# Kernel optimization log

Hardware: AMD Instinct MI355X
Metric: run time of the kernel (lower is better)

## Reference

```python
import jax, jax.numpy as jnp
import numpy as np

B, S, T = 64, 1024, 64
H, A, DA, DT, P, NT = 1024, 1024, 512, 256, 256, 32
DIN = DA + A + DT  # LSTMCell input: [a_tm1_embed, att_tm1, pre_type]


def setup_inputs() -> dict:
    key = jax.random.key(0)
    ks = jax.random.split(key, 16)
    nrm = lambda k, shape, s=0.02: jax.random.normal(k, shape, jnp.float32) * s
    return {
        'src_encodings': jax.random.normal(ks[0], (B, S, H), jnp.float32),
        'W_ih': nrm(ks[1], (4 * H, DIN)), 'b_ih': jnp.zeros((4 * H,), jnp.float32),
        'W_hh': nrm(ks[2], (4 * H, H)), 'b_hh': jnp.zeros((4 * H,), jnp.float32),
        'W_att': nrm(ks[3], (H, H)),            # att_sketch_linear (no bias)
        'W_attvec': nrm(ks[4], (A, 2 * H)),     # sketch_att_vec_linear (no bias)
        'W_init': nrm(ks[5], (H, H)), 'b_init': jnp.zeros((H,), jnp.float32),  # decoder_cell_init
        'W_q2a': nrm(ks[6], (DA, A)), 'b_q2a': jnp.zeros((DA,), jnp.float32),  # query_vec_to_action_embed
        'prod_embed': nrm(ks[7], (P, DA), 0.05), 'prod_bias': jnp.zeros((P,), jnp.float32),
        'type_embed': nrm(ks[8], (NT, DT), 0.05),
        'prev_prod_ids': jax.random.randint(ks[9], (B, T), 0, P),
        'prev_type_ids': jax.random.randint(ks[10], (B, T), 0, NT),
        'target_prod_ids': jax.random.randint(ks[11], (B, T), 0, P),
        'sketch_lens': jax.random.randint(ks[12], (B,), T // 2, T + 1),
        'src_lens': jax.random.randint(ks[13], (B,), S // 2, S + 1),
    }


def _lstm_cell(x, h, c, W_ih, b_ih, W_hh, b_hh):
    gates = x @ W_ih.T + b_ih + h @ W_hh.T + b_hh
    i, f, g, o = jnp.split(gates, 4, axis=-1)
    c_new = jax.nn.sigmoid(f) * c + jax.nn.sigmoid(i) * jnp.tanh(g)
    h_new = jax.nn.sigmoid(o) * jnp.tanh(c_new)
    return h_new, c_new


def reference(src_encodings, W_ih, b_ih, W_hh, b_hh, W_att, W_attvec, W_init, b_init,
              W_q2a, b_q2a, prod_embed, prod_bias, type_embed,
              prev_prod_ids, prev_type_ids, target_prod_ids, sketch_lens, src_lens):
    Bq, Sq, Hq = src_encodings.shape
    Tq = prev_prod_ids.shape[1]
    src_valid = jnp.arange(Sq)[None, :] < src_lens[:, None]            # [B,S] True = real token
    step_valid = jnp.arange(Tq)[None, :] < sketch_lens[:, None]        # [B,T]
    prev_valid = step_valid & (jnp.arange(Tq)[None, :] > 0)            # prev action exists

    src_att = jnp.einsum('bsh,kh->bsk', src_encodings, W_att)          # att_sketch_linear
    # init_decoder_state(adaptive_avg_pool1d(enc,1))
    init_cell = src_encodings.mean(axis=1)
    h0 = jnp.tanh(init_cell @ W_init.T + b_init)
    c0 = jnp.zeros_like(h0)
    att0 = jnp.zeros((Bq, A), src_encodings.dtype)

    # precomputed grammar lookups (production / type embeddings of a_{t-1})
    a_embeds = jnp.where(prev_valid[..., None], prod_embed[prev_prod_ids], 0.0)   # [B,T,DA]
    t_embeds = jnp.where(prev_valid[..., None], type_embed[prev_type_ids], 0.0)   # [B,T,DT]
    is_first = jnp.arange(Tq) == 0                                                # [T]

    def step(carry, inp):
        h, c, att_tm1 = carry
        a_e, t_e, first = inp
        x = jnp.concatenate([a_e, att_tm1, t_e], axis=-1)
        x = jnp.where(first, 0.0, x)                                   # t==0 -> zero input
        h, c = _lstm_cell(x, h, c, W_ih, b_ih, W_hh, b_hh)
        scores = jnp.einsum('bh,bsh->bs', h, src_att)
        scores = jnp.where(src_valid, scores, -1e9)
        alpha = jax.nn.softmax(scores, axis=-1)
        ctx = jnp.einsum('bs,bsh->bh', alpha, src_encodings)
        att_t = jnp.tanh(jnp.concatenate([h, ctx], axis=-1) @ W_attvec.T)
        q = jnp.tanh(att_t @ W_q2a.T + b_q2a)                          # non_linear readout
        probs = jax.nn.softmax(q @ prod_embed.T + prod_bias, axis=-1)  # [B,P]
        return (h, c, att_t), probs

    xs = (jnp.swapaxes(a_embeds, 0, 1), jnp.swapaxes(t_embeds, 0, 1), is_first)
    _, probs = jax.lax.scan(step, (h0, c0, att0), xs)                  # [T,B,P]

    tgt = jnp.swapaxes(target_prod_ids, 0, 1)[..., None]               # [T,B,1]
    p_t = jnp.take_along_axis(probs, tgt, axis=-1)[..., 0]             # [T,B]
    logp = jnp.log(p_t + 1e-8)
    sketch_prob = jnp.sum(jnp.where(step_valid.T, logp, 0.0), axis=0)  # [B]
    return sketch_prob
```

## Files before the change

### kernel.cpp

```cpp
#include <hip/hip_runtime.h>
#include <hip/hip_bf16.h>

typedef unsigned short u16;
typedef unsigned char u8;
typedef unsigned int u32;
typedef unsigned long long u64;
typedef __attribute__((ext_vector_type(8))) short short8;
typedef __attribute__((ext_vector_type(8))) u16 ushort8;
typedef __attribute__((ext_vector_type(4))) float f32x4;
typedef __attribute__((ext_vector_type(2))) float f32x2;

__device__ __forceinline__ float bf2f(u16 x){ u32 u=((u32)x)<<16; return __builtin_bit_cast(float,u); }
__device__ __forceinline__ u16 f2bf(float f){ u32 u=__builtin_bit_cast(u32,f); u32 r=(u+0x7fffu+((u>>16)&1u))>>16; return (u16)r; }
__device__ __forceinline__ float sigf(float x){ return 1.f/(1.f+__expf(-x)); }

__device__ __forceinline__ void scf(float* p, float v){
  __hip_atomic_store(p, v, __ATOMIC_RELAXED, __HIP_MEMORY_SCOPE_AGENT);
}
__device__ __forceinline__ void scu16(u16* p, u16 v){
  __hip_atomic_store(p, v, __ATOMIC_RELAXED, __HIP_MEMORY_SCOPE_AGENT);
}
__device__ __forceinline__ int ald(const int* p){
  return __hip_atomic_load(p, __ATOMIC_RELAXED, __HIP_MEMORY_SCOPE_AGENT);
}


__global__ __launch_bounds__(256) void k_cast(const float* __restrict__ s, u16* __restrict__ d, long n){
  long i = ((long)blockIdx.x*256 + threadIdx.x)*8;
  if (i >= n) return;
  float4 a = *(const float4*)(s+i);
  float4 b = *(const float4*)(s+i+4);
  ushort8 o;
  o[0]=f2bf(a.x); o[1]=f2bf(a.y); o[2]=f2bf(a.z); o[3]=f2bf(a.w);
  o[4]=f2bf(b.x); o[5]=f2bf(b.y); o[6]=f2bf(b.z); o[7]=f2bf(b.w);
  *(ushort8*)(d+i) = o;
}

__global__ __launch_bounds__(256) void k_cast8(const float* __restrict__ s, u8* __restrict__ d, long n){
  long i = ((long)blockIdx.x*256 + threadIdx.x)*8;
  if (i >= n) return;
  float4 a = *(const float4*)(s+i);
  float4 b = *(const float4*)(s+i+4);
  u32 w0 = 0, w1 = 0;
  w0 = __builtin_amdgcn_cvt_pk_fp8_f32(a.x, a.y, w0, false);
  w0 = __builtin_amdgcn_cvt_pk_fp8_f32(a.z, a.w, w0, true);
  w1 = __builtin_amdgcn_cvt_pk_fp8_f32(b.x, b.y, w1, false);
  w1 = __builtin_amdgcn_cvt_pk_fp8_f32(b.z, b.w, w1, true);
  uint2 o; o.x = w0; o.y = w1;
  *(uint2*)(d+i) = o;
}

__global__ __launch_bounds__(256) void k_build_wc(const float* __restrict__ Wih, const float* __restrict__ Whh,
                                                  u16* __restrict__ WC){
  long i8 = (long)blockIdx.x*256 + threadIdx.x;
  if (i8 >= (long)4096*352) return;
  int j = (int)(i8/352); int kk = (int)(i8%352)*8;
  const float* src;
  if (kk < 512)        src = Wih + (long)j*1792 + kk;
  else if (kk < 768)   src = Wih + (long)j*1792 + (kk+1024);
  else if (kk < 1792)  src = Wih + (long)j*1792 + (kk-256);
  else                 src = Whh + (long)j*1024 + (kk-1792);
  u16* dst = WC + (long)j*2816 + kk;
  ushort8 o;
  #pragma unroll
  for (int q=0;q<8;++q) o[q] = f2bf(src[q]);
  *(ushort8*)dst = o;
}

__global__ __launch_bounds__(256) void k_wattT(const float* __restrict__ Wa, u16* __restrict__ WT){
  int id = blockIdx.x*256 + threadIdx.x;
  int m = id >> 10, k = id & 1023;
  WT[(long)m*1024 + k] = f2bf(Wa[(long)k*1024 + m]);
}

__global__ __launch_bounds__(256) void k_meanf(const float* __restrict__ enc, u16* __restrict__ MEANB){
  int b = blockIdx.x, h = blockIdx.y*256 + threadIdx.x;
  const float* p = enc + ((long)b<<20) + h;
  float s = 0.f;
  for (int ss=0; ss<1024; ++ss) s += p[(long)ss<<10];
  MEANB[b*1024 + h] = f2bf(s * (1.f/1024.f));
}

__global__ __launch_bounds__(256) void k_embed(const float* __restrict__ pemb, const float* __restrict__ temb,
      const int* __restrict__ pid, const int* __restrict__ tid_, const int* __restrict__ slen,
      u16* __restrict__ XC){
  int t = blockIdx.x >> 6, b = blockIdx.x & 63;
  bool valid = (t>0) && (t < slen[b]);
  int pi = pid[b*64 + t], ti = tid_[b*64 + t];
  u16* dst = XC + (long)blockIdx.x*2816;
  for (int kk = threadIdx.x; kk < 768; kk += 256){
    float v = 0.f;
    if (valid) v = (kk<512) ? pemb[(long)pi*512 + kk] : temb[(long)ti*256 + (kk-512)];
    dst[kk] = f2bf(v);
  }
}

template<int MODE>
__global__ __launch_bounds__(256) void k_gemm(const u16* __restrict__ A, long lda,
      const u16* __restrict__ W, int K, const float* __restrict__ bias,
      float* __restrict__ OF, long ldo, u16* __restrict__ OB1, long ldb1){
  int l = threadIdx.x & 63, w = threadIdx.x >> 6;
  int c = l & 15, g = l >> 4;
  int n0 = blockIdx.x*16, m0 = blockIdx.y*64;
  const u16* ap = A + (long)(m0 + w*16 + c)*lda + g*8;
  const u16* bp = W + (long)(n0 + c)*K + g*8;
  f32x4 acc = {0.f,0.f,0.f,0.f};
  int kit = K >> 5;
  #pragma unroll 4
  for (int kb=0; kb<kit; ++kb){
    short8 av = *(const short8*)(ap + kb*32);
    short8 bv = *(const short8*)(bp + kb*32);
    acc = __builtin_amdgcn_mfma_f32_16x16x32_bf16(av, bv, acc, 0, 0, 0);
  }
  #pragma unroll
  for (int r=0;r<4;++r){
    int row = m0 + w*16 + g*4 + r;
    int col = n0 + c;
    float v = acc[r];
    if (MODE==2){ OB1[(long)row*ldb1 + col] = f2bf(tanhf(v + bias[col])); }
    if (MODE==3){ OF[(long)row*ldo + col] = v + bias[col]; }
  }
}

__global__ __launch_bounds__(256) void k_loss(const float* __restrict__ LG, const int* __restrict__ tgt,
      const int* __restrict__ slen, float* __restrict__ out){
  int b = blockIdx.x;
  int w = threadIdx.x >> 6, l = threadIdx.x & 63;
  int len = slen[b];
  float accum = 0.f;
  for (int t = w; t < 64; t += 4){
    if (t >= len) continue;
    const float* lp = LG + ((long)(t*64 + b))*256;
    float v0=lp[l], v1=lp[l+64], v2=lp[l+128], v3=lp[l+192];
    float mx = fmaxf(fmaxf(v0,v1), fmaxf(v2,v3));
    #pragma unroll
    for (int off=32; off; off>>=1) mx = fmaxf(mx, __shfl_xor(mx, off));
    float s = __expf(v0-mx)+__expf(v1-mx)+__expf(v2-mx)+__expf(v3-mx);
    #pragma unroll
    for (int off=32; off; off>>=1) s += __shfl_xor(s, off);
    float ltg = lp[tgt[b*64 + t]];
    float p = __expf(ltg - mx)/s;
    accum += logf(p + 1e-8f);
  }
  __shared__ float sm[4];
  if (l == 0) sm[w] = accum;
  __syncthreads();
  if (threadIdx.x == 0) out[b] = sm[0]+sm[1]+sm[2]+sm[3];
}

__device__ __forceinline__ void gbar(int* __restrict__ BAR, int gen){
  int grp = blockIdx.x & 15;
  int prev = __hip_atomic_fetch_add(BAR + grp*16, 1, __ATOMIC_RELAXED, __HIP_MEMORY_SCOPE_AGENT);
  if (prev == gen*16 - 1){
    int p2 = __hip_atomic_fetch_add(BAR + 256, 1, __ATOMIC_RELAXED, __HIP_MEMORY_SCOPE_AGENT);
    if (p2 == gen*16 - 1){
      #pragma unroll
      for (int i=0;i<16;++i)
        __hip_atomic_store(BAR + 320 + i*16, gen, __ATOMIC_RELAXED, __HIP_MEMORY_SCOPE_AGENT);
    }
  }
  while (ald(BAR + 320 + grp*16) < gen)
    __builtin_amdgcn_s_sleep(2);
}

__global__ __launch_bounds__(1024,1) void k_decoder(
      const u8* __restrict__ ENC8, const u16* __restrict__ WC,
      const u16* __restrict__ WAVT, const u16* __restrict__ WAVEC,
      const float* __restrict__ bih, const float* __restrict__ bhh,
      u16* __restrict__ XC, u16* __restrict__ ATT,
      float* __restrict__ HWT, float* __restrict__ PLT,
      u16* __restrict__ CTXBT, const int* __restrict__ src_lens,
      int* __restrict__ BAR){
  const int tid = threadIdx.x;
  const int w = tid >> 6, l = tid & 63, c = l & 15, g = l >> 4;
  const int bx = blockIdx.x;
  int genb = 0;

  __shared__ float smem[12320];
  f32x4* lacc  = (f32x4*)smem;
  float* s_ctx = smem;
  float* s_ls  = smem + 12288;
  u16*   ldsc  = (u16*)smem;
  f32x4* lacc4 = (f32x4*)(smem + 8192);

  const int n0 = bx << 2;
  const int jrow = n0 + (c & 3) + ((c >> 2) << 10);
  const float biasj = bih[jrow] + bhh[jrow];
  const int kh = w >> 2, mt = w & 3;
  const int lbase = l & 0x33;
  float creg[4] = {0.f,0.f,0.f,0.f};
  const int mt2 = bx & 3, nt2 = bx >> 2;
  const int b3 = bx >> 2, ci3 = bx & 3;
  int len3 = src_lens[b3]; if (len3 < 1) len3 = 1; if (len3 > 1024) len3 = 1024;
  const int chunk3 = (len3 + 3) >> 2;
  int s0 = ci3*chunk3;
  int s1 = s0 + chunk3; if (s1 > len3) s1 = len3;
  const u8* encb = ENC8 + (((long)b3)<<20);
  int lim = s1 - s0 - w;
  int nqv = (lim <= 0) ? 0 : ((lim + 15) >> 4);
  if (nqv > 16) nqv = 16;
  const int mt4 = bx & 3, nt4 = bx >> 2;
  const int b16 = tid >> 6, lane64 = tid & 63;

  uint4 er[12];
  #pragma unroll
  for (int q=0;q<12;++q){
    int r = s0 + q*16 + w;
    if (r >= s1) r = s0;
    er[q] = *(const uint4*)(encb + ((long)r<<10) + l*16);
  }

  for (int t = 0; t < 64; ++t){
    const u16* XCt = XC + (size_t)t*64*2816;
    u16* XCn = XC + (size_t)(t+1)*64*2816;
    const u16* Hcur = XCn + 1792;
    float* HW   = HWT  + ((size_t)t<<16);
    float* PL   = PLT  + ((size_t)t<<8);
    u16*  CTXB  = CTXBT + ((size_t)t<<18);

    {
      const u16* ap = XCt + (long)(mt*16 + c)*2816 + kh*704 + g*8;
      const u16* bp = WC  + (long)jrow*2816 + kh*704 + g*8;
      f32x4 acc = {0.f,0.f,0.f,0.f};
      #pragma unroll 11
      for (int kb=0; kb<22; ++kb){
        short8 av = *(const short8*)(ap + kb*32);
        short8 bv = *(const short8*)(bp + kb*32);
        acc = __builtin_amdgcn_mfma_f32_16x16x32_bf16(av, bv, acc, 0, 0, 0);
      }
      lacc[w*64 + l] = acc;
      __syncthreads();
      if (w < 4){
        f32x4 a0 = lacc[w*64 + l];
        f32x4 a1 = lacc[(w+4)*64 + l];
        f32x4 a2 = lacc[(w+8)*64 + l];
        f32x4 a3 = lacc[(w+12)*64 + l];
        #pragma unroll
        for (int r=0;r<4;++r){
          float val = a0[r] + a1[r] + a2[r] + a3[r] + biasj;
          float iv = __shfl(val, lbase);
          float fv = __shfl(val, lbase+4);
          float gv = __shfl(val, lbase+8);
          float ov = __shfl(val, lbase+12);
          if ((l & 12) == 0){
            float cn = sigf(fv)*creg[r] + sigf(iv)*tanhf(gv);
            float hn = sigf(ov)*tanhf(cn);
            creg[r] = cn;
            int b = w*16 + g*4 + r;
            int n = n0 + (l & 3);
            scu16(XCn + (long)b*2816 + 1792 + n, f2bf(hn));
          }
        }
      }
    }
    ++genb;
    __syncthreads();
    if (tid == 0) gbar(BAR, genb);
    __syncthreads();

    {
      const u16* ap = Hcur + (long)(mt2*16 + c)*2816 + w*64 + g*8;
      const u16* bp = WAVT + (long)(nt2*16 + c)*1024 + w*64 + g*8;
      f32x4 acc = {0.f,0.f,0.f,0.f};
      #pragma unroll
      for (int kb=0; kb<2; ++kb){
        short8 av = *(const short8*)(ap + kb*32);
        short8 bv = *(const short8*)(bp + kb*32);
        acc = __builtin_amdgcn_mfma_f32_16x16x32_bf16(av, bv, acc, 0, 0, 0);
      }
      lacc[w*64 + l] = acc;
      __syncthreads();
      if (w == 0){
        f32x4 rd = lacc[l];
        #pragma unroll
        for (int w2=1; w2<16; ++w2) rd += lacc[w2*64 + l];
        #pragma unroll
        for (int r=0;r<4;++r)
          scf(HW + (long)(mt2*16 + g*4 + r)*1024 + nt2*16 + c, rd[r]);
      }
    }
    ++genb;
    __syncthreads();
    if (tid == 0) gbar(BAR, genb);
    __syncthreads();

    {
      float hw[16], ctx[16];
      const float* hwp = HW + b3*1024 + l*16;
      #pragma unroll
      for (int jj=0;jj<4;++jj){
        float4 v = *(const float4*)(hwp + jj*4);
        hw[4*jj]=v.x; hw[4*jj+1]=v.y; hw[4*jj+2]=v.z; hw[4*jj+3]=v.w;
      }
      #pragma unroll
      for (int jj=0;jj<16;++jj) ctx[jj]=0.f;
      float lsum = 0.f;
      auto proc = [&](uint4 ev){
        float e[16];
        #pragma unroll
        for (int jj=0;jj<4;++jj){
          u32 x = ((const u32*)&ev)[jj];
          f32x2 lo = __builtin_amdgcn_cvt_pk_f32_fp8(x, false);
          f32x2 hi = __builtin_amdgcn_cvt_pk_f32_fp8(x, true);
          e[4*jj]=lo[0]; e[4*jj+1]=lo[1]; e[4*jj+2]=hi[0]; e[4*jj+3]=hi[1];
        }
        float sc = 0.f;
        #pragma unroll
        for (int jj=0;jj<16;++jj) sc += e[jj]*hw[jj];
        #pragma unroll
        for (int off=32; off; off>>=1) sc += __shfl_xor(sc, off);
        float pe = __expf(sc);
        lsum += pe;
        #pragma unroll
        for (int jj=0;jj<16;++jj) ctx[jj] += pe*e[jj];
      };
      #pragma unroll
      for (int q=0;q<12;++q) if (q < nqv) proc(er[q]);
      for (int q=12; q<nqv; ++q){
        uint4 ev = *(const uint4*)(encb + ((long)(s0 + q*16 + w)<<10) + l*16);
        proc(ev);
      }
      if (l == 0) s_ls[w] = lsum;
      if (w < 8){
        #pragma unroll
        for (int jj=0;jj<16;++jj) s_ctx[w*1024 + l*16 + jj] = ctx[jj];
      }
      __syncthreads();
      if (w >= 8){
        #pragma unroll
        for (int jj=0;jj<16;++jj) s_ctx[(w-8)*1024 + l*16 + jj] += ctx[jj];
      }
      __syncthreads();
      {
        float v = 0.f;
        #pragma unroll
        for (int p=0;p<8;++p) v += s_ctx[p*1024 + tid];
        scu16(CTXB + (((long)bx)<<10) + tid, f2bf(v));
      }
      if (tid == 0){
        float L = 0.f;
        #pragma unroll
        for (int q=0;q<16;++q) L += s_ls[q];
        scf(PL + bx, L);
      }
    }
    ++genb;
    __syncthreads();
    if (tid == 0) gbar(BAR, genb);
    __syncthreads();

    {
      int b = mt4*16 + b16;
      float L = PL[b*4] + PL[b*4+1] + PL[b*4+2] + PL[b*4+3];
      float inv = (L > 0.f) ? 1.f/L : 0.f;
      const u16* r0 = CTXB + (long)(b*4+0)*1024;
      const u16* r1 = CTXB + (long)(b*4+1)*1024;
      const u16* r2 = CTXB + (long)(b*4+2)*1024;
      const u16* r3 = CTXB + (long)(b*4+3)*1024;
      const int swz = (b16 & 7) << 3;
      #pragma unroll
      for (int q=0;q<2;++q){
        int mcol8 = (lane64 + q*64)*8;
        ushort8 v0 = *(const ushort8*)(r0 + mcol8);
        ushort8 v1 = *(const ushort8*)(r1 + mcol8);
        ushort8 v2 = *(const ushort8*)(r2 + mcol8);
        ushort8 v3 = *(const ushort8*)(r3 + mcol8);
        ushort8 o;
        #pragma unroll
        for (int j=0;j<8;++j)
          o[j] = f2bf((bf2f(v0[j]) + bf2f(v1[j]) + bf2f(v2[j]) + bf2f(v3[j])) * inv);
        *(ushort8*)(ldsc + ((b16*1024 + mcol8) ^ swz)) = o;
      }
      __syncthreads();
      f32x4 acc = {0.f,0.f,0.f,0.f};
      const int koff = (w < 8) ? w*128 : 1024 + (w-8)*128;
      const u16* bp = WAVEC + (long)(nt4*16 + c)*2048 + koff + g*8;
      if (w < 8){
        const u16* ap = Hcur + (long)(mt4*16 + c)*2816 + w*128 + g*8;
        #pragma unroll
        for (int kb=0; kb<4; ++kb){
          short8 av = *(const short8*)(ap + kb*32);
          short8 bv = *(const short8*)(bp + kb*32);
          acc = __builtin_amdgcn_mfma_f32_16x16x32_bf16(av, bv, acc, 0, 0, 0);
        }
      } else {
        const int cswz = (c & 7) << 3;
        const int kbase = c*1024 + (w-8)*128 + g*8;
        #pragma unroll
        for (int kb=0; kb<4; ++kb){
          short8 av = *(const short8*)(ldsc + ((kbase + kb*32) ^ cswz));
          short8 bv = *(const short8*)(bp + kb*32);
          acc = __builtin_amdgcn_mfma_f32_16x16x32_bf16(av, bv, acc, 0, 0, 0);
        }
      }
      lacc4[w*64 + l] = acc;
      __syncthreads();
      if (w == 0){
        f32x4 rd = lacc4[l];
        #pragma unroll
        for (int w2=1; w2<16; ++w2) rd += lacc4[w2*64 + l];
        #pragma unroll
        for (int r=0;r<4;++r){
          int b_ = mt4*16 + g*4 + r;
          int col = nt4*16 + c;
          u16 x = f2bf(tanhf(rd[r]));
          scu16(XCn + (long)b_*2816 + 768 + col, x);
          ATT[((long)t*64 + b_)*1024 + col] = x;
        }
      }
    }
    ++genb;
    __syncthreads();
    if (tid == 0) gbar(BAR, genb);
    __syncthreads();
  }
}

extern "C" void kernel_launch(void* const* d_in, const int* in_sizes, int n_in,
                              void* d_out, int out_size, void* d_ws, size_t ws_size,
                              hipStream_t stream){
  const float* enc      = (const float*)d_in[0];
  const float* W_ih     = (const float*)d_in[1];
  const float* b_ih     = (const float*)d_in[2];
  const float* W_hh     = (const float*)d_in[3];
  const float* b_hh     = (const float*)d_in[4];
  const float* W_att    = (const float*)d_in[5];
  const float* W_attvec = (const float*)d_in[6];
  const float* W_init   = (const float*)d_in[7];
  const float* b_init   = (const float*)d_in[8];
  const float* W_q2a    = (const float*)d_in[9];
  const float* b_q2a    = (const float*)d_in[10];
  const float* prod_emb = (const float*)d_in[11];
  const float* prod_bias= (const float*)d_in[12];
  const float* type_emb = (const float*)d_in[13];
  const int* prev_pid   = (const int*)d_in[14];
  const int* prev_tid   = (const int*)d_in[15];
  const int* target     = (const int*)d_in[16];
  const int* sk_lens    = (const int*)d_in[17];
  const int* src_lens   = (const int*)d_in[18];
  float* out = (float*)d_out;

  char* ws = (char*)d_ws;
  size_t o = 0;
  auto alloc = [&](size_t bytes)->char*{ char* p = ws + o; o += (bytes + 255) & ~(size_t)255; return p; };
  u8*   ENC8 = (u8*)alloc((size_t)64*1024*1024);
  u16*  WC   = (u16*)alloc((size_t)4096*2816*2);
  u16*  WAVT = (u16*)alloc((size_t)1024*1024*2);
  u16*  WAVEC= (u16*)alloc((size_t)1024*2048*2);
  u16*  WQ   = (u16*)alloc((size_t)512*1024*2);
  u16*  PE   = (u16*)alloc((size_t)256*512*2);
  u16*  WINIT= (u16*)alloc((size_t)1024*1024*2);
  u16*  MEANB= (u16*)alloc((size_t)64*1024*2);
  u16*  XC   = (u16*)alloc((size_t)65*64*2816*2);
  u16*  ATT  = (u16*)alloc((size_t)64*64*1024*2);
  float* HWT = (float*)alloc((size_t)64*64*1024*4);
  float* PLT = (float*)alloc((size_t)64*256*4);
  u16*  CTXBT=(u16*)alloc((size_t)64*256*1024*2);
  u16*  Q    = (u16*)alloc((size_t)4096*512*2);
  float* LG  = (float*)alloc((size_t)4096*256*4);
  int*  BAR  = (int*)alloc(4096);
  (void)ws_size; (void)in_sizes; (void)n_in; (void)out_size;

  hipMemsetAsync(XC, 0, (size_t)64*2816*2, stream);
  hipMemsetAsync(BAR, 0, 4096, stream);

  k_cast8<<<32768,256,0,stream>>>(enc, ENC8, (long)64*1024*1024);
  k_cast<<<1024,256,0,stream>>>(W_attvec, WAVEC, (long)1024*2048);
  k_cast<<<256,256,0,stream>>>(W_q2a, WQ, (long)512*1024);
  k_cast<<<64,256,0,stream>>>(prod_emb, PE, (long)256*512);
  k_cast<<<512,256,0,stream>>>(W_init, WINIT, (long)1024*1024);
  k_build_wc<<<5632,256,0,stream>>>(W_ih, W_hh, WC);
  k_wattT<<<4096,256,0,stream>>>(W_att, WAVT);
  k_meanf<<<dim3(64,4),256,0,stream>>>(enc, MEANB);
  k_gemm<2><<<dim3(64,1),256,0,stream>>>(MEANB, 1024L, WINIT, 1024, b_init,
                                         nullptr, 0L, XC + 1792, 2816L);
  k_embed<<<4096,256,0,stream>>>(prod_emb, type_emb, prev_pid, prev_tid, sk_lens, XC);

  k_decoder<<<256,1024,0,stream>>>(ENC8, WC, WAVT, WAVEC, b_ih, b_hh,
                                   XC, ATT, HWT, PLT, CTXBT, src_lens, BAR);

  k_gemm<2><<<dim3(32,64),256,0,stream>>>(ATT, 1024L, WQ, 1024, b_q2a,
                                          nullptr, 0L, Q, 512L);
  k_gemm<3><<<dim3(16,64),256,0,stream>>>(Q, 512L, PE, 512, prod_bias,
                                          LG, 256L, nullptr, 0L);
  k_loss<<<64,256,0,stream>>>(LG, target, sk_lens, out);
}
```

Baseline: 3.868 ms.

## Partition decoder blocks into four batch groups with independent 64-block barriers

Reassigns work so each group of 64 blocks owns 16 batch rows end to end (LSTM gates, attention projection, context, attention vector), which lets the grid barrier be replaced by four independent 64-block barriers instead of one 256-block barrier. The aim is to cut barrier latency and contention per step. In exchange, each block now reads the full weight rows for its slice while handling fewer batch rows, so the weights are read four times as often. The attention output store also becomes an atomic relaxed store.

```diff
diff --git a/kernel.cpp b/kernel.cpp
--- a/kernel.cpp
+++ b/kernel.cpp
@@ -148,18 +148,18 @@
   if (threadIdx.x == 0) out[b] = sm[0]+sm[1]+sm[2]+sm[3];
 }
 
-__device__ __forceinline__ void gbar(int* __restrict__ BAR, int gen){
-  int grp = blockIdx.x & 15;
-  int prev = __hip_atomic_fetch_add(BAR + grp*16, 1, __ATOMIC_RELAXED, __HIP_MEMORY_SCOPE_AGENT);
-  if (prev == gen*16 - 1){
-    int p2 = __hip_atomic_fetch_add(BAR + 256, 1, __ATOMIC_RELAXED, __HIP_MEMORY_SCOPE_AGENT);
-    if (p2 == gen*16 - 1){
-      #pragma unroll
-      for (int i=0;i<16;++i)
-        __hip_atomic_store(BAR + 320 + i*16, gen, __ATOMIC_RELAXED, __HIP_MEMORY_SCOPE_AGENT);
+__device__ __forceinline__ void gbar64(int* __restrict__ B, int gen, int sub){
+  int g8 = sub & 7;
+  int prev = __hip_atomic_fetch_add(B + g8*16, 1, __ATOMIC_RELAXED, __HIP_MEMORY_SCOPE_AGENT);
+  if (prev == gen*8 - 1){
+    int p2 = __hip_atomic_fetch_add(B + 128, 1, __ATOMIC_RELAXED, __HIP_MEMORY_SCOPE_AGENT);
+    if (p2 == gen*8 - 1){
+      #pragma unroll
+      for (int i=0;i<8;++i)
+        __hip_atomic_store(B + 160 + i*16, gen, __ATOMIC_RELAXED, __HIP_MEMORY_SCOPE_AGENT);
     }
   }
-  while (ald(BAR + 320 + grp*16) < gen)
+  while (ald(B + 160 + g8*16) < gen)
     __builtin_amdgcn_s_sleep(2);
 }
 
@@ -174,6 +174,8 @@
   const int tid = threadIdx.x;
   const int w = tid >> 6, l = tid & 63, c = l & 15, g = l >> 4;
   const int bx = blockIdx.x;
+  const int grpid = bx >> 6, sub = bx & 63, bg0 = grpid << 4;
+  int* BARg = BAR + grpid*1024;
   int genb = 0;
 
   __shared__ float smem[12320];
@@ -183,14 +185,12 @@
   u16*   ldsc  = (u16*)smem;
   f32x4* lacc4 = (f32x4*)(smem + 8192);
 
-  const int n0 = bx << 2;
-  const int jrow = n0 + (c & 3) + ((c >> 2) << 10);
+  const int ns = w & 3, kh = w >> 2;
+  const int jrow = sub*16 + ns*4 + (c & 3) + ((c >> 2) << 10);
   const float biasj = bih[jrow] + bhh[jrow];
-  const int kh = w >> 2, mt = w & 3;
   const int lbase = l & 0x33;
   float creg[4] = {0.f,0.f,0.f,0.f};
-  const int mt2 = bx & 3, nt2 = bx >> 2;
-  const int b3 = bx >> 2, ci3 = bx & 3;
+  const int b3 = bg0 + (sub >> 2), ci3 = sub & 3;
   int len3 = src_lens[b3]; if (len3 < 1) len3 = 1; if (len3 > 1024) len3 = 1024;
   const int chunk3 = (len3 + 3) >> 2;
   int s0 = ci3*chunk3;
@@ -199,7 +199,6 @@
   int lim = s1 - s0 - w;
   int nqv = (lim <= 0) ? 0 : ((lim + 15) >> 4);
   if (nqv > 16) nqv = 16;
-  const int mt4 = bx & 3, nt4 = bx >> 2;
   const int b16 = tid >> 6, lane64 = tid & 63;
 
   uint4 er[12];
@@ -219,7 +218,7 @@
     u16*  CTXB  = CTXBT + ((size_t)t<<18);
 
     {
-      const u16* ap = XCt + (long)(mt*16 + c)*2816 + kh*704 + g*8;
+      const u16* ap = XCt + (long)(bg0 + c)*2816 + kh*704 + g*8;
       const u16* bp = WC  + (long)jrow*2816 + kh*704 + g*8;
       f32x4 acc = {0.f,0.f,0.f,0.f};
       #pragma unroll 11
@@ -246,8 +245,8 @@
             float cn = sigf(fv)*creg[r] + sigf(iv)*tanhf(gv);
             float hn = sigf(ov)*tanhf(cn);
             creg[r] = cn;
-            int b = w*16 + g*4 + r;
-            int n = n0 + (l & 3);
+            int b = bg0 + g*4 + r;
+            int n = sub*16 + w*4 + (l & 3);
             scu16(XCn + (long)b*2816 + 1792 + n, f2bf(hn));
           }
         }
@@ -255,12 +254,12 @@
     }
     ++genb;
     __syncthreads();
-    if (tid == 0) gbar(BAR, genb);
+    if (tid == 0) gbar64(BARg, genb, sub);
     __syncthreads();
 
     {
-      const u16* ap = Hcur + (long)(mt2*16 + c)*2816 + w*64 + g*8;
-      const u16* bp = WAVT + (long)(nt2*16 + c)*1024 + w*64 + g*8;
+      const u16* ap = Hcur + (long)(bg0 + c)*2816 + w*64 + g*8;
+      const u16* bp = WAVT + (long)(sub*16 + c)*1024 + w*64 + g*8;
       f32x4 acc = {0.f,0.f,0.f,0.f};
       #pragma unroll
       for (int kb=0; kb<2; ++kb){
@@ -276,17 +275,17 @@
         for (int w2=1; w2<16; ++w2) rd += lacc[w2*64 + l];
         #pragma unroll
         for (int r=0;r<4;++r)
-          scf(HW + (long)(mt2*16 + g*4 + r)*1024 + nt2*16 + c, rd[r]);
+          scf(HW + (long)(bg0 + g*4 + r)*1024 + sub*16 + c, rd[r]);
       }
     }
     ++genb;
     __syncthreads();
-    if (tid == 0) gbar(BAR, genb);
+    if (tid == 0) gbar64(BARg, genb, sub);
     __syncthreads();
 
     {
       float hw[16], ctx[16];
-      const float* hwp = HW + b3*1024 + l*16;
+      const float* hwp = HW + (long)b3*1024 + l*16;
       #pragma unroll
       for (int jj=0;jj<4;++jj){
         float4 v = *(const float4*)(hwp + jj*4);
@@ -346,17 +345,18 @@
     }
     ++genb;
     __syncthreads();
-    if (tid == 0) gbar(BAR, genb);
+    if (tid == 0) gbar64(BARg, genb, sub);
     __syncthreads();
 
     {
-      int b = mt4*16 + b16;
-      float L = PL[b*4] + PL[b*4+1] + PL[b*4+2] + PL[b*4+3];
+      int pb = grpid*64 + b16*4;
+      float4 plv = *(const float4*)(PL + pb);
+      float L = plv.x + plv.y + plv.z + plv.w;
       float inv = (L > 0.f) ? 1.f/L : 0.f;
-      const u16* r0 = CTXB + (long)(b*4+0)*1024;
-      const u16* r1 = CTXB + (long)(b*4+1)*1024;
-      const u16* r2 = CTXB + (long)(b*4+2)*1024;
-      const u16* r3 = CTXB + (long)(b*4+3)*1024;
+      const u16* r0 = CTXB + ((long)(pb+0)<<10);
+      const u16* r1 = CTXB + ((long)(pb+1)<<10);
+      const u16* r2 = CTXB + ((long)(pb+2)<<10);
+      const u16* r3 = CTXB + ((long)(pb+3)<<10);
       const int swz = (b16 & 7) << 3;
       #pragma unroll
       for (int q=0;q<2;++q){
@@ -374,9 +374,9 @@
       __syncthreads();
       f32x4 acc = {0.f,0.f,0.f,0.f};
       const int koff = (w < 8) ? w*128 : 1024 + (w-8)*128;
-      const u16* bp = WAVEC + (long)(nt4*16 + c)*2048 + koff + g*8;
+      const u16* bp = WAVEC + (long)(sub*16 + c)*2048 + koff + g*8;
       if (w < 8){
-        const u16* ap = Hcur + (long)(mt4*16 + c)*2816 + w*128 + g*8;
+        const u16* ap = Hcur + (long)(bg0 + c)*2816 + w*128 + g*8;
         #pragma unroll
         for (int kb=0; kb<4; ++kb){
           short8 av = *(const short8*)(ap + kb*32);
@@ -401,17 +401,17 @@
         for (int w2=1; w2<16; ++w2) rd += lacc4[w2*64 + l];
         #pragma unroll
         for (int r=0;r<4;++r){
-          int b_ = mt4*16 + g*4 + r;
-          int col = nt4*16 + c;
+          int b_ = bg0 + g*4 + r;
+          int col = sub*16 + c;
           u16 x = f2bf(tanhf(rd[r]));
           scu16(XCn + (long)b_*2816 + 768 + col, x);
-          ATT[((long)t*64 + b_)*1024 + col] = x;
+          scu16(ATT + ((long)t*64 + b_)*1024 + col, x);
         }
       }
     }
     ++genb;
     __syncthreads();
-    if (tid == 0) gbar(BAR, genb);
+    if (tid == 0) gbar64(BARg, genb, sub);
     __syncthreads();
   }
 }
@@ -458,11 +458,11 @@
   u16*  CTXBT=(u16*)alloc((size_t)64*256*1024*2);
   u16*  Q    = (u16*)alloc((size_t)4096*512*2);
   float* LG  = (float*)alloc((size_t)4096*256*4);
-  int*  BAR  = (int*)alloc(4096);
+  int*  BAR  = (int*)alloc(16384);
   (void)ws_size; (void)in_sizes; (void)n_in; (void)out_size;
 
   hipMemsetAsync(XC, 0, (size_t)64*2816*2, stream);
-  hipMemsetAsync(BAR, 0, 4096, stream);
+  hipMemsetAsync(BAR, 0, 16384, stream);
 
   k_cast8<<<32768,256,0,stream>>>(enc, ENC8, (long)64*1024*1024);
   k_cast<<<1024,256,0,stream>>>(W_attvec, WAVEC, (long)1024*2048);
```

Measured after the change: 3.886 ms. About the same (+0.4%).

## Assign attention blocks to batches in proportion to source length

Applied to the files above, without the earlier changes.

A new single-thread setup kernel gives each batch row between 1 and 8 of the 256 decoder blocks, in proportion to its source length, instead of a fixed 4 blocks per row. The attention step splits sequence chunks using this table, and the context reduction now sums a variable number of partial rows (up to 8). The aim is to balance work per block so the slowest block, which every grid barrier waits on, has fewer rows. The cost is an extra tiny kernel, indirect table lookups, and a reduction that always loads 8 rows where it used to load 4.

```diff
diff --git a/kernel.cpp b/kernel.cpp
--- a/kernel.cpp
+++ b/kernel.cpp
@@ -92,6 +92,27 @@
     float v = 0.f;
     if (valid) v = (kk<512) ? pemb[(long)pi*512 + kk] : temb[(long)ti*256 + (kk-512)];
     dst[kk] = f2bf(v);
+  }
+}
+
+__global__ void k_assign(const int* __restrict__ slen, int* __restrict__ ASG){
+  if (threadIdx.x != 0 || blockIdx.x != 0) return;
+  int lenv[64]; long total = 0;
+  for (int b=0;b<64;++b){ int L = slen[b]; if (L<1)L=1; if (L>1024)L=1024; lenv[b]=L; total+=L; }
+  int cnt[64]; int sum=0;
+  for (int b=0;b<64;++b){
+    int c = (int)(((long)256*lenv[b])/total);
+    if (c<1)c=1; if (c>8)c=8; cnt[b]=c; sum+=c;
+  }
+  int rem = 256 - sum; int bi = 0;
+  while (rem > 0){ if (cnt[bi&63] < 8){ cnt[bi&63]++; rem--; } bi++; }
+  while (rem < 0){ if (cnt[bi&63] > 1){ cnt[bi&63]--; rem++; } bi++; }
+  int st = 0;
+  for (int b=0;b<64;++b){
+    ASG[1024+b] = cnt[b];
+    ASG[1088+b] = st;
+    for (int i=0;i<cnt[b];++i){ ASG[st+i] = b; ASG[256+st+i] = i; }
+    st += cnt[b];
   }
 }
 
@@ -170,7 +191,7 @@
       u16* __restrict__ XC, u16* __restrict__ ATT,
       float* __restrict__ HWT, float* __restrict__ PLT,
       u16* __restrict__ CTXBT, const int* __restrict__ src_lens,
-      int* __restrict__ BAR){
+      const int* __restrict__ ASG, int* __restrict__ BAR){
   const int tid = threadIdx.x;
   const int w = tid >> 6, l = tid & 63, c = l & 15, g = l >> 4;
   const int bx = blockIdx.x;
@@ -190,11 +211,13 @@
   const int lbase = l & 0x33;
   float creg[4] = {0.f,0.f,0.f,0.f};
   const int mt2 = bx & 3, nt2 = bx >> 2;
-  const int b3 = bx >> 2, ci3 = bx & 3;
+  const int b3 = ASG[bx];
+  const int ci3 = ASG[256 + bx];
+  const int nch3 = ASG[1024 + b3];
   int len3 = src_lens[b3]; if (len3 < 1) len3 = 1; if (len3 > 1024) len3 = 1024;
-  const int chunk3 = (len3 + 3) >> 2;
+  const int chunk3 = (len3 + nch3 - 1)/nch3;
   int s0 = ci3*chunk3;
-  int s1 = s0 + chunk3; if (s1 > len3) s1 = len3;
+  int s1 = s0 + chunk3; if (s1 > len3) s1 = len3; if (s0 > s1) s0 = s1;
   const u8* encb = ENC8 + (((long)b3)<<20);
   int lim = s1 - s0 - w;
   int nqv = (lim <= 0) ? 0 : ((lim + 15) >> 4);
@@ -351,24 +374,46 @@
 
     {
       int b = mt4*16 + b16;
-      float L = PL[b*4] + PL[b*4+1] + PL[b*4+2] + PL[b*4+3];
+      int st = ASG[1088 + b], nL = ASG[1024 + b];
+      float plv[8];
+      #pragma unroll
+      for (int p=0;p<8;++p){ int ip = st + ((p<nL)? p:0); plv[p] = PL[ip]; }
+      float L = 0.f;
+      #pragma unroll
+      for (int p=0;p<8;++p) if (p<nL) L += plv[p];
       float inv = (L > 0.f) ? 1.f/L : 0.f;
-      const u16* r0 = CTXB + (long)(b*4+0)*1024;
-      const u16* r1 = CTXB + (long)(b*4+1)*1024;
-      const u16* r2 = CTXB + (long)(b*4+2)*1024;
-      const u16* r3 = CTXB + (long)(b*4+3)*1024;
+      float acc16[16];
+      #pragma unroll
+      for (int q=0;q<16;++q) acc16[q] = 0.f;
+      #pragma unroll
+      for (int rnd=0; rnd<2; ++rnd){
+        ushort8 va[4][2];
+        #pragma unroll
+        for (int q4=0;q4<4;++q4){
+          int p = rnd*4+q4; int ip = st + ((p<nL)? p:0);
+          const u16* row = CTXB + (((long)ip)<<10);
+          va[q4][0] = *(const ushort8*)(row + lane64*8);
+          va[q4][1] = *(const ushort8*)(row + (lane64+64)*8);
+        }
+        #pragma unroll
+        for (int q4=0;q4<4;++q4){
+          int p = rnd*4+q4;
+          if (p<nL){
+            #pragma unroll
+            for (int j=0;j<8;++j){
+              acc16[j]   += bf2f(va[q4][0][j]);
+              acc16[8+j] += bf2f(va[q4][1][j]);
+            }
+          }
+        }
+      }
       const int swz = (b16 & 7) << 3;
       #pragma unroll
       for (int q=0;q<2;++q){
         int mcol8 = (lane64 + q*64)*8;
-        ushort8 v0 = *(const ushort8*)(r0 + mcol8);
-        ushort8 v1 = *(const ushort8*)(r1 + mcol8);
-        ushort8 v2 = *(const ushort8*)(r2 + mcol8);
-        ushort8 v3 = *(const ushort8*)(r3 + mcol8);
         ushort8 o;
         #pragma unroll
-        for (int j=0;j<8;++j)
-          o[j] = f2bf((bf2f(v0[j]) + bf2f(v1[j]) + bf2f(v2[j]) + bf2f(v3[j])) * inv);
+        for (int j=0;j<8;++j) o[j] = f2bf(acc16[q*8+j]*inv);
         *(ushort8*)(ldsc + ((b16*1024 + mcol8) ^ swz)) = o;
       }
       __syncthreads();
@@ -405,7 +450,7 @@
           int col = nt4*16 + c;
           u16 x = f2bf(tanhf(rd[r]));
           scu16(XCn + (long)b_*2816 + 768 + col, x);
-          ATT[((long)t*64 + b_)*1024 + col] = x;
+          scu16(ATT + ((long)t*64 + b_)*1024 + col, x);
         }
       }
     }
@@ -459,11 +504,13 @@
   u16*  Q    = (u16*)alloc((size_t)4096*512*2);
   float* LG  = (float*)alloc((size_t)4096*256*4);
   int*  BAR  = (int*)alloc(4096);
+  int*  ASG  = (int*)alloc(8192);
   (void)ws_size; (void)in_sizes; (void)n_in; (void)out_size;
 
   hipMemsetAsync(XC, 0, (size_t)64*2816*2, stream);
   hipMemsetAsync(BAR, 0, 4096, stream);
 
+  k_assign<<<1,64,0,stream>>>(src_lens, ASG);
   k_cast8<<<32768,256,0,stream>>>(enc, ENC8, (long)64*1024*1024);
   k_cast<<<1024,256,0,stream>>>(W_attvec, WAVEC, (long)1024*2048);
   k_cast<<<256,256,0,stream>>>(W_q2a, WQ, (long)512*1024);
@@ -477,7 +524,7 @@
   k_embed<<<4096,256,0,stream>>>(prod_emb, type_emb, prev_pid, prev_tid, sk_lens, XC);
 
   k_decoder<<<256,1024,0,stream>>>(ENC8, WC, WAVT, WAVEC, b_ih, b_hh,
-                                   XC, ATT, HWT, PLT, CTXBT, src_lens, BAR);
+                                   XC, ATT, HWT, PLT, CTXBT, src_lens, ASG, BAR);
 
   k_gemm<2><<<dim3(32,64),256,0,stream>>>(ATT, 1024L, WQ, 1024, b_q2a,
                                           nullptr, 0L, Q, 512L);
```

Result: slower. 4.223 ms (+9.2%).
